# Kernel optimization log

Measured on AMD Instinct MI355X. Metric: run time of the kernel, lower is better.

## Reference

```python
import jax, jax.numpy as jnp
import numpy as np

D = 1024      # hidden_dim
H = 16        # num_heads
KV = 8        # num_kv_heads
HD = D // H   # head_size = 64
M = 3584      # intermediate_dim
E = 8         # num_local_experts
TOPK = 2      # num_experts_per_tok
EPS = 1e-6
ROPE_THETA = 10000.0


def setup_inputs() -> dict:
    key = jax.random.key(0)
    ks = jax.random.split(key, 12)
    s = 0.02
    B, S = 2, 1024
    return {
        "x": jax.random.normal(ks[0], (B, S, D), jnp.float32),
        "ln1_w": jnp.ones((D,), jnp.float32),
        "ln2_w": jnp.ones((D,), jnp.float32),
        "wq": jax.random.normal(ks[1], (D, H * HD), jnp.float32) * s,
        "wk": jax.random.normal(ks[2], (D, KV * HD), jnp.float32) * s,
        "wv": jax.random.normal(ks[3], (D, KV * HD), jnp.float32) * s,
        "wo": jax.random.normal(ks[4], (H * HD, D), jnp.float32) * s,
        "router_w": jax.random.normal(ks[5], (D, E), jnp.float32) * s,
        "w_gate": jax.random.normal(ks[6], (E, D, M), jnp.float32) * s,
        "w_up": jax.random.normal(ks[7], (E, D, M), jnp.float32) * s,
        "w_down": jax.random.normal(ks[8], (E, M, D), jnp.float32) * s,
    }


def _rmsnorm(x, w, eps=EPS):
    xf = x.astype(jnp.float32)
    var = jnp.mean(xf * xf, axis=-1, keepdims=True)
    return (xf * jax.lax.rsqrt(var + eps)).astype(x.dtype) * w


def _rope(q, k):
    # q: [B,S,H,HD], k: [B,S,KV,HD]
    S = q.shape[1]
    inv_freq = 1.0 / (ROPE_THETA ** (jnp.arange(0, HD, 2, dtype=jnp.float32) / HD))
    ang = jnp.arange(S, dtype=jnp.float32)[:, None] * inv_freq[None, :]  # [S, HD/2]
    cos = jnp.concatenate([jnp.cos(ang), jnp.cos(ang)], axis=-1)[None, :, None, :]
    sin = jnp.concatenate([jnp.sin(ang), jnp.sin(ang)], axis=-1)[None, :, None, :]

    def rot_half(t):
        t1, t2 = jnp.split(t, 2, axis=-1)
        return jnp.concatenate([-t2, t1], axis=-1)

    return q * cos + rot_half(q) * sin, k * cos + rot_half(k) * sin


def reference(x, ln1_w, ln2_w, wq, wk, wv, wo, router_w, w_gate, w_up, w_down):
    B, S, _ = x.shape

    # ---- self-attention block ----
    h = _rmsnorm(x, ln1_w)
    q = (h @ wq).reshape(B, S, H, HD)
    k = (h @ wk).reshape(B, S, KV, HD)
    v = (h @ wv).reshape(B, S, KV, HD)
    q, k = _rope(q, k)
    rep = H // KV
    k = jnp.repeat(k, rep, axis=2)  # [B,S,H,HD]
    v = jnp.repeat(v, rep, axis=2)
    scores = jnp.einsum("bqhd,bkhd->bhqk", q, k) / jnp.sqrt(jnp.float32(HD))
    causal = jnp.tril(jnp.ones((S, S), bool))
    scores = jnp.where(causal[None, None], scores, jnp.finfo(scores.dtype).min)
    attn = jax.nn.softmax(scores, axis=-1)
    ao = jnp.einsum("bhqk,bkhd->bqhd", attn, v).reshape(B, S, H * HD)
    x = x + ao @ wo

    # ---- sparse MoE block (top-2 routing, SwiGLU experts) ----
    h = _rmsnorm(x, ln2_w)
    logits = h @ router_w                       # [B,S,E]
    probs = jax.nn.softmax(logits, axis=-1)
    topv, topi = jax.lax.top_k(probs, TOPK)     # [B,S,K]
    topv = topv / jnp.sum(topv, axis=-1, keepdims=True)
    # dense combine weights [B,S,E]: zero for unselected experts
    weights = jnp.sum(jax.nn.one_hot(topi, E, dtype=h.dtype) * topv[..., None], axis=-2)
    gate = jnp.einsum("bsd,edm->bsem", h, w_gate)
    up = jnp.einsum("bsd,edm->bsem", h, w_up)
    act = jax.nn.silu(gate) * up * weights[..., None]
    moe = jnp.einsum("bsem,emd->bsd", act, w_down)
    return x + moe
```

## Files before the change

kernel.cpp:

```cpp
#include <hip/hip_runtime.h>

typedef __attribute__((ext_vector_type(8))) short short8;
typedef __attribute__((ext_vector_type(4))) float f32x4;
typedef unsigned int u32;

#define DI static __device__ __forceinline__

DI unsigned short f2bf(float f) {
  unsigned u = __builtin_bit_cast(unsigned, f);
  u += 0x7fffu + ((u >> 16) & 1u);
  return (unsigned short)(u >> 16);
}
DI float bf2f(unsigned short b) {
  unsigned u = ((unsigned)b) << 16;
  return __builtin_bit_cast(float, u);
}

DI void gload16(const unsigned short* g, unsigned short* l) {
  __builtin_amdgcn_global_load_lds(
      (const __attribute__((address_space(1))) u32*)g,
      (__attribute__((address_space(3))) u32*)l, 16, 0, 0);
}

static constexpr int NT   = 2048;
static constexpr int SEQ  = 1024;
static constexpr int DIM  = 1024;
static constexpr int NH   = 16;
static constexpr int NKV  = 8;
static constexpr int HD   = 64;
static constexpr int MDIM = 3584;
static constexpr int NE   = 8;
static constexpr int QW   = 2048;
static constexpr int GUW  = 2 * MDIM;

template <int ROWMAP>
__global__ void __launch_bounds__(256) transpose_kernel(
    const float* __restrict__ in, unsigned short* __restrict__ out,
    int R, int C, size_t in_estride, size_t out_estride) {
  __shared__ unsigned short tl[64][66];
  int e = blockIdx.z;
  const float* ip = in + (size_t)e * in_estride;
  unsigned short* op = out + (size_t)e * out_estride;
  int c0 = blockIdx.x * 64, r0 = blockIdx.y * 64;
  int tid = threadIdx.x;
  {
    int lr = tid >> 4, lc = (tid & 15) * 4;
#pragma unroll
    for (int p = 0; p < 4; ++p) {
      int r = p * 16 + lr;
      float4 v = *(const float4*)(ip + (size_t)(r0 + r) * C + c0 + lc);
      tl[lc + 0][r] = f2bf(v.x);
      tl[lc + 1][r] = f2bf(v.y);
      tl[lc + 2][r] = f2bf(v.z);
      tl[lc + 3][r] = f2bf(v.w);
    }
  }
  __syncthreads();
  {
    int c = tid >> 2, rc = (tid & 3) * 16;
    unsigned short tmp[16];
#pragma unroll
    for (int j = 0; j < 8; ++j) {
      u32 w = *(const u32*)&tl[c][rc + j * 2];
      tmp[j * 2] = (unsigned short)w;
      tmp[j * 2 + 1] = (unsigned short)(w >> 16);
    }
    int cg = c0 + c;
    int orow;
    if (ROWMAP == 0) orow = cg;
    else orow = ((cg >> 4) << 5) + (cg & 15) + (ROWMAP == 2 ? 16 : 0);
    unsigned short* dst = op + (size_t)orow * R + r0 + rc;
#pragma unroll
    for (int j = 0; j < 2; ++j)
      *(uint4*)(dst + j * 8) = *(const uint4*)&tmp[j * 8];
  }
}

__global__ void __launch_bounds__(256) vtrans_kernel(const unsigned short* __restrict__ qkv,
                                                     unsigned short* __restrict__ vT) {
  __shared__ unsigned short tl[64][66];
  int s0 = blockIdx.x * 64;
  int kvh = blockIdx.y;
  int b = blockIdx.z;
  int tid = threadIdx.x;
  {
    int r = tid >> 2, cc = (tid & 3) * 16;
    const unsigned short* src =
        qkv + ((size_t)(b * SEQ + s0 + r)) * QW + (DIM + NKV * HD + kvh * HD) + cc;
    unsigned short tmp[16];
    *(uint4*)&tmp[0] = *(const uint4*)src;
    *(uint4*)&tmp[8] = *(const uint4*)(src + 8);
#pragma unroll
    for (int j = 0; j < 16; ++j) tl[cc + j][r] = tmp[j];
  }
  __syncthreads();
  {
    int h = tid >> 2, sc = (tid & 3) * 16;
    unsigned short o[16];
#pragma unroll
    for (int j = 0; j < 16; ++j) o[j] = tl[h][sc + j];
    unsigned short* dst = vT + (((size_t)(b * NKV + kvh) * HD + h) * SEQ) + s0 + sc;
    *(uint4*)dst = *(const uint4*)&o[0];
    *(uint4*)(dst + 8) = *(const uint4*)&o[8];
  }
}

__global__ void __launch_bounds__(256) rmsnorm_kernel(const float* __restrict__ x,
                                                      const float* __restrict__ w,
                                                      unsigned short* __restrict__ out) {
  int row = blockIdx.x;
  const float* xr = x + (size_t)row * DIM;
  int i = threadIdx.x * 4;
  float4 v = *(const float4*)(xr + i);
  float s = v.x * v.x + v.y * v.y + v.z * v.z + v.w * v.w;
  for (int o = 32; o; o >>= 1) s += __shfl_xor(s, o);
  __shared__ float red[4];
  if ((threadIdx.x & 63) == 0) red[threadIdx.x >> 6] = s;
  __syncthreads();
  s = red[0] + red[1] + red[2] + red[3];
  float r = rsqrtf(s * (1.0f / DIM) + 1e-6f);
  float4 wv = *(const float4*)(w + i);
  ushort4 o4;
  o4.x = f2bf(v.x * r * wv.x);
  o4.y = f2bf(v.y * r * wv.y);
  o4.z = f2bf(v.z * r * wv.z);
  o4.w = f2bf(v.w * r * wv.w);
  *(ushort4*)(out + (size_t)row * DIM + i) = o4;
}

template <int GATHER, int EPI>
__global__ void __launch_bounds__(256) gemmT_kernel(
    const unsigned short* __restrict__ A, int lda,
    const unsigned short* __restrict__ B, int ldb, size_t b_estride,
    void* __restrict__ Cv, int ldc,
    const float* __restrict__ resid,
    int M, int K,
    const int* __restrict__ lists, const int* __restrict__ cnt,
    int ks_count, size_t ks_stride) {
  constexpr int BN = 128;
  constexpr int NBLK = 2;
  int zz = blockIdx.z;
  int e = zz / ks_count, ks = zz - e * ks_count;
  int KL = K / ks_count;
  int kbase = ks * KL;

  int count = M;
  const int* lst = nullptr;
  if (GATHER != 0) {
    count = cnt[e];
    if (count <= 0) return;
    lst = lists + e * NT;
    B += b_estride * (size_t)e;
  }
  int m0 = blockIdx.y * 128;
  if (m0 >= count) return;
  int n0 = blockIdx.x * BN;

  __shared__ unsigned short sB[3][BN * 32];

  int tid = threadIdx.x, w = tid >> 6, lane = tid & 63;
  int l15 = lane & 15, lhi = lane >> 4;
  int wm = w >> 1, wn = w & 1;

  int srow = w * 16 + (lane >> 2);
  int schunk = (((lane & 3) - ((lane >> 3) & 3)) & 3) * 8;
  const unsigned short* bSrc[NBLK];
#pragma unroll
  for (int s = 0; s < NBLK; ++s)
    bSrc[s] = B + (size_t)(n0 + s * 64 + srow) * ldb + kbase + schunk;
  unsigned ldst = (unsigned)(w * 16) * 32;

  auto stage = [&](int buf, int k0) {
#pragma unroll
    for (int s = 0; s < NBLK; ++s)
      gload16(bSrc[s] + k0, &sB[buf][ldst + s * 64 * 32]);
  };

  const unsigned short* aFrag[4];
#pragma unroll
  for (int mi = 0; mi < 4; ++mi) {
    int mr = m0 + wm * 64 + mi * 16 + l15;
    if (mr > count - 1) mr = count - 1;
    int ar;
    if (GATHER == 0) ar = mr;
    else {
      int pid = lst[mr];
      ar = (GATHER == 1) ? (pid >> 1) : pid;
    }
    aFrag[mi] = A + (size_t)ar * lda + kbase + lhi * 8;
  }

  f32x4 acc[4][4] = {};
  int fslot = ((lhi + (l15 >> 1)) & 3) * 8;
  int boff[4];
#pragma unroll
  for (int t = 0; t < 4; ++t) {
    int col = wn * 64 + t * 16 + l15;
    boff[t] = col * 32 + fslot;
  }

  int nsteps = KL / 32;
  int cur = 0, stg = 2;

  short8 afA[4], afB[4];
  stage(0, 0);
  stage(1, 32);
#pragma unroll
  for (int mi = 0; mi < 4; ++mi) afA[mi] = *(const short8*)(aFrag[mi]);

  auto body = [&](int T, short8(&C)[4], short8(&N)[4]) {
    if (T + 1 < nsteps) asm volatile("s_waitcnt vmcnt(6)" ::: "memory");
    else                asm volatile("s_waitcnt vmcnt(4)" ::: "memory");
    __builtin_amdgcn_s_barrier();
    __builtin_amdgcn_sched_barrier(0);
    int tn = (T + 1 < nsteps) ? T + 1 : T;
#pragma unroll
    for (int mi = 0; mi < 4; ++mi)
      N[mi] = *(const short8*)(aFrag[mi] + (size_t)tn * 32);
    if (T + 2 < nsteps) stage(stg, (T + 2) * 32);
    const unsigned short* pb = sB[cur];
    short8 bfr[4];
#pragma unroll
    for (int q = 0; q < 4; ++q) bfr[q] = *(const short8*)&pb[boff[q]];
    __builtin_amdgcn_s_setprio(1);
#pragma unroll
    for (int mi = 0; mi < 4; ++mi)
#pragma unroll
      for (int ni = 0; ni < 4; ++ni)
        acc[mi][ni] =
            __builtin_amdgcn_mfma_f32_16x16x32_bf16(C[mi], bfr[ni], acc[mi][ni], 0, 0, 0);
    __builtin_amdgcn_s_setprio(0);
    cur = (cur == 2) ? 0 : cur + 1;
    stg = (stg == 2) ? 0 : stg + 1;
  };

  for (int t = 0; t < nsteps; t += 2) {
    body(t, afA, afB);
    body(t + 1, afB, afA);
  }

#pragma unroll
  for (int mi = 0; mi < 4; ++mi) {
#pragma unroll
    for (int r = 0; r < 4; ++r) {
      int mr = m0 + wm * 64 + mi * 16 + lhi * 4 + r;
      if (GATHER != 0 && mr >= count) continue;
      size_t crow = (GATHER != 0) ? (size_t)lst[mr] : (size_t)mr;
      if (EPI == 3) {
        float wgt = resid[crow];
        int colbase = (n0 + wn * 64) >> 1;
#pragma unroll
        for (int ni = 0; ni < 4; ni += 2) {
          float g = acc[mi][ni][r], u = acc[mi][ni + 1][r];
          float sv = g / (1.f + __expf(-g));
          ((unsigned short*)Cv)[crow * ldc + colbase + (ni >> 1) * 16 + l15] =
              f2bf(sv * u * wgt);
        }
      } else {
#pragma unroll
        for (int ni = 0; ni < 4; ++ni) {
          int n = n0 + wn * 64 + ni * 16 + l15;
          float val = acc[mi][ni][r];
          if (EPI == 0)
            ((unsigned short*)Cv)[crow * ldc + n] = f2bf(val);
          else if (EPI == 1)
            ((float*)Cv)[crow * ldc + n] = val + resid[crow * ldc + n];
          else
            ((float*)Cv)[(size_t)ks * ks_stride + crow * ldc + n] = val;
        }
      }
    }
  }
}

__global__ void __launch_bounds__(256) rope_kernel(unsigned short* __restrict__ qkv) {
  int g = blockIdx.x * 256 + threadIdx.x;
  int i = g & 31;
  int hh = (g >> 5) % (NH + NKV);
  int tok = g / (32 * (NH + NKV));
  if (tok >= NT) return;
  int s = tok & (SEQ - 1);
  float inv = exp2f((float)i * (-13.287712379549449f / 32.0f));
  float ang = (float)s * inv;
  float sn = sinf(ang);
  float c = cosf(ang);
  int col = (hh < NH) ? hh * HD : DIM + (hh - NH) * HD;
  unsigned short* ptr = qkv + (size_t)tok * QW + col;
  float a = bf2f(ptr[i]), b2 = bf2f(ptr[i + 32]);
  ptr[i] = f2bf(a * c - b2 * sn);
  ptr[i + 32] = f2bf(b2 * c + a * sn);
}

__global__ void __launch_bounds__(64) attn_kernel(const unsigned short* __restrict__ qkv,
                                                  const unsigned short* __restrict__ vT,
                                                  unsigned short* __restrict__ ao) {
  __shared__ unsigned short Ps[16 * 64];
  int bid = blockIdx.x;
  int qt = bid & 63;
  int h = (bid >> 6) & 15;
  int b = bid >> 10;
  int lane = threadIdx.x, l15 = lane & 15, lhi = lane >> 4;
  int q0 = qt * 16, kvh = h >> 1;
  int kcol = DIM + kvh * HD;

  const unsigned short* qp = qkv + ((size_t)(b * SEQ + q0 + l15)) * QW + h * HD + lhi * 8;
  short8 aq0 = *(const short8*)qp;
  short8 aq1 = *(const short8*)(qp + 32);

  const unsigned short* vbase = vT + ((size_t)(b * NKV + kvh) * HD) * SEQ;

  float m[4] = {-1e30f, -1e30f, -1e30f, -1e30f};
  float l[4] = {0.f, 0.f, 0.f, 0.f};
  f32x4 accO[4] = {};

  int nkb = (qt >> 2) + 1;
  for (int kb_ = 0; kb_ < nkb; ++kb_) {
    int kbase = kb_ * 64;
    f32x4 s[4];
#pragma unroll
    for (int ct = 0; ct < 4; ++ct) {
      const unsigned short* kp =
          qkv + ((size_t)(b * SEQ + kbase + ct * 16 + l15)) * QW + kcol + lhi * 8;
      short8 k0v = *(const short8*)kp;
      short8 k1v = *(const short8*)(kp + 32);
      f32x4 a = {};
      a = __builtin_amdgcn_mfma_f32_16x16x32_bf16(aq0, k0v, a, 0, 0, 0);
      a = __builtin_amdgcn_mfma_f32_16x16x32_bf16(aq1, k1v, a, 0, 0, 0);
      int kpos = kbase + ct * 16 + l15;
#pragma unroll
      for (int r = 0; r < 4; ++r) {
        float v = a[r] * 0.125f;
        if (kpos > q0 + lhi * 4 + r) v = -1e30f;
        s[ct][r] = v;
      }
    }
    float nm[4], al[4], rs[4];
#pragma unroll
    for (int r = 0; r < 4; ++r) {
      float mb = fmaxf(fmaxf(s[0][r], s[1][r]), fmaxf(s[2][r], s[3][r]));
      mb = fmaxf(mb, __shfl_xor(mb, 1));
      mb = fmaxf(mb, __shfl_xor(mb, 2));
      mb = fmaxf(mb, __shfl_xor(mb, 4));
      mb = fmaxf(mb, __shfl_xor(mb, 8));
      nm[r] = fmaxf(m[r], mb);
      al[r] = __expf(m[r] - nm[r]);
      m[r] = nm[r];
      rs[r] = 0.f;
    }
#pragma unroll
    for (int ct = 0; ct < 4; ++ct) {
#pragma unroll
      for (int r = 0; r < 4; ++r) {
        float p = __expf(s[ct][r] - nm[r]);
        rs[r] += p;
        int q = lhi * 4 + r;
        Ps[q * 64 + ((ct * 16 + l15) ^ (lhi << 4))] = f2bf(p);
      }
    }
#pragma unroll
    for (int r = 0; r < 4; ++r) {
      rs[r] += __shfl_xor(rs[r], 1);
      rs[r] += __shfl_xor(rs[r], 2);
      rs[r] += __shfl_xor(rs[r], 4);
      rs[r] += __shfl_xor(rs[r], 8);
      l[r] = l[r] * al[r] + rs[r];
    }
#pragma unroll
    for (int dt = 0; dt < 4; ++dt)
#pragma unroll
      for (int r = 0; r < 4; ++r) accO[dt][r] *= al[r];

    int pswz = (l15 >> 2) << 4;
    short8 ap0 = *(const short8*)&Ps[l15 * 64 + ((lhi * 8) ^ pswz)];
    short8 ap1 = *(const short8*)&Ps[l15 * 64 + ((32 + lhi * 8) ^ pswz)];
#pragma unroll
    for (int dt = 0; dt < 4; ++dt) {
#pragma unroll
      for (int ks = 0; ks < 2; ++ks) {
        const unsigned short* vp =
            vbase + ((size_t)(dt * 16 + l15)) * SEQ + kbase + ks * 32 + lhi * 8;
        short8 vf = *(const short8*)vp;
        accO[dt] = __builtin_amdgcn_mfma_f32_16x16x32_bf16(ks ? ap1 : ap0, vf, accO[dt], 0, 0, 0);
      }
    }
  }
  float invl[4];
#pragma unroll
  for (int r = 0; r < 4; ++r) invl[r] = 1.f / l[r];
#pragma unroll
  for (int dt = 0; dt < 4; ++dt)
#pragma unroll
    for (int r = 0; r < 4; ++r)
      ao[((size_t)(b * SEQ + q0 + lhi * 4 + r)) * DIM + h * HD + dt * 16 + l15] =
          f2bf(accO[dt][r] * invl[r]);
}

__global__ void zero_cnt_kernel(int* __restrict__ cnt) {
  if (threadIdx.x < NE) cnt[threadIdx.x] = 0;
}

__global__ void __launch_bounds__(64) router_kernel(const float* __restrict__ x2,
                                                    const float* __restrict__ ln2w,
                                                    const float* __restrict__ rw,
                                                    float* __restrict__ wts,
                                                    int* __restrict__ cnt,
                                                    int* __restrict__ lists) {
  int t = blockIdx.x, lane = threadIdx.x;
  const float* xr = x2 + (size_t)t * DIM;
  float xs[16];
  double ssq = 0.0;
#pragma unroll
  for (int j = 0; j < 16; ++j) {
    xs[j] = xr[lane + j * 64];
    ssq += (double)xs[j] * xs[j];
  }
  for (int o = 32; o; o >>= 1) ssq += __shfl_xor(ssq, o);
  double r = rsqrt(ssq * (1.0 / DIM) + 1e-6);
  double p[NE] = {};
#pragma unroll
  for (int j = 0; j < 16; ++j) {
    int i = lane + j * 64;
    double hv = (double)xs[j] * r * (double)ln2w[i];
    const float* rwp = rw + (size_t)i * NE;
#pragma unroll
    for (int e = 0; e < NE; ++e) p[e] += hv * (double)rwp[e];
  }
  for (int o = 32; o; o >>= 1) {
#pragma unroll
    for (int e = 0; e < NE; ++e) p[e] += __shfl_xor(p[e], o);
  }
  if (lane == 0) {
    int i1 = 0;
    for (int e = 1; e < NE; ++e)
      if (p[e] > p[i1]) i1 = e;
    int i2 = (i1 == 0) ? 1 : 0;
    for (int e = 0; e < NE; ++e)
      if (e != i1 && p[e] > p[i2]) i2 = e;
    double mx = fmax(p[i1], p[i2]);
    double e1 = exp(p[i1] - mx), e2 = exp(p[i2] - mx);
    double inv = 1.0 / (e1 + e2);
    wts[t * 2] = (float)(e1 * inv);
    wts[t * 2 + 1] = (float)(e2 * inv);
    int pos1 = atomicAdd(&cnt[i1], 1);
    lists[i1 * NT + pos1] = t * 2;
    int pos2 = atomicAdd(&cnt[i2], 1);
    lists[i2 * NT + pos2] = t * 2 + 1;
  }
}

__global__ void __launch_bounds__(256) combine_kernel(const float* __restrict__ x2,
                                                      const float* __restrict__ part,
                                                      float* __restrict__ out) {
  const size_t KSS = (size_t)2 * NT * DIM;
  size_t idx = ((size_t)blockIdx.x * 256 + threadIdx.x) * 4;
  size_t t = idx >> 10;
  size_t d = idx & 1023;
  float4 o = *(const float4*)(x2 + idx);
#pragma unroll
  for (int s = 0; s < 4; ++s) {
    float4 b0 = *(const float4*)(part + s * KSS + (t * 2) * DIM + d);
    float4 c0 = *(const float4*)(part + s * KSS + (t * 2 + 1) * DIM + d);
    o.x += b0.x + c0.x;
    o.y += b0.y + c0.y;
    o.z += b0.z + c0.z;
    o.w += b0.w + c0.w;
  }
  *(float4*)(out + idx) = o;
}

extern "C" void kernel_launch(void* const* d_in, const int* in_sizes, int n_in,
                              void* d_out, int out_size, void* d_ws, size_t ws_size,
                              hipStream_t stream) {
  const float* x   = (const float*)d_in[0];
  const float* ln1 = (const float*)d_in[1];
  const float* ln2 = (const float*)d_in[2];
  const float* wq  = (const float*)d_in[3];
  const float* wk  = (const float*)d_in[4];
  const float* wv  = (const float*)d_in[5];
  const float* wo  = (const float*)d_in[6];
  const float* rw  = (const float*)d_in[7];
  const float* wg  = (const float*)d_in[8];
  const float* wu  = (const float*)d_in[9];
  const float* wd  = (const float*)d_in[10];
  float* out = (float*)d_out;

  char* p = (char*)d_ws;
  auto take = [&](size_t bytes) {
    char* q = p;
    p += (bytes + 255) & ~(size_t)255;
    return q;
  };
  unsigned short* wguT = (unsigned short*)take((size_t)NE * GUW * DIM * 2);
  unsigned short* wdT  = (unsigned short*)take((size_t)NE * DIM * MDIM * 2);
  float*          x2   = (float*)take((size_t)NT * DIM * 4);
  unsigned short* h2   = (unsigned short*)take((size_t)NT * DIM * 2);
  float*          part = (float*)take((size_t)4 * 2 * NT * DIM * 4);
  unsigned short* act  = (unsigned short*)take((size_t)2 * NT * MDIM * 2);
  float*          wtsb = (float*)take((size_t)2 * NT * 4);
  int*            cntb = (int*)take(NE * 4);
  int*            listsb = (int*)take((size_t)NE * NT * 4);
  char* X = p;
  unsigned short* wqkvT = (unsigned short*)X;
  unsigned short* woT   = wqkvT + (size_t)QW * DIM;
  unsigned short* h1    = woT + (size_t)DIM * DIM;
  unsigned short* qkv   = h1 + (size_t)NT * DIM;
  unsigned short* aob   = qkv + (size_t)NT * QW;
  unsigned short* vT    = aob + (size_t)NT * DIM;

  transpose_kernel<0><<<dim3(16, 16, 1), 256, 0, stream>>>(wq, wqkvT, DIM, DIM, 0, 0);
  transpose_kernel<0><<<dim3(8, 16, 1), 256, 0, stream>>>(wk, wqkvT + (size_t)DIM * DIM, DIM, 512, 0, 0);
  transpose_kernel<0><<<dim3(8, 16, 1), 256, 0, stream>>>(wv, wqkvT + (size_t)(DIM + 512) * DIM, DIM, 512, 0, 0);
  transpose_kernel<0><<<dim3(16, 16, 1), 256, 0, stream>>>(wo, woT, DIM, DIM, 0, 0);
  transpose_kernel<1><<<dim3(56, 16, NE), 256, 0, stream>>>(
      wg, wguT, DIM, MDIM, (size_t)DIM * MDIM, (size_t)GUW * DIM);
  transpose_kernel<2><<<dim3(56, 16, NE), 256, 0, stream>>>(
      wu, wguT, DIM, MDIM, (size_t)DIM * MDIM, (size_t)GUW * DIM);
  transpose_kernel<0><<<dim3(16, 56, NE), 256, 0, stream>>>(
      wd, wdT, MDIM, DIM, (size_t)MDIM * DIM, (size_t)DIM * MDIM);

  rmsnorm_kernel<<<NT, 256, 0, stream>>>(x, ln1, h1);
  gemmT_kernel<0, 0><<<dim3(QW / 128, NT / 128, 1), 256, 0, stream>>>(
      h1, DIM, wqkvT, DIM, 0, qkv, QW, nullptr, NT, DIM, nullptr, nullptr, 1, 0);
  rope_kernel<<<(NT * (NH + NKV) * 32) / 256, 256, 0, stream>>>(qkv);
  vtrans_kernel<<<dim3(SEQ / 64, NKV, 2), 256, 0, stream>>>(qkv, vT);
  attn_kernel<<<NT * NH / 16, 64, 0, stream>>>(qkv, vT, aob);
  gemmT_kernel<0, 1><<<dim3(DIM / 128, NT / 128, 1), 256, 0, stream>>>(
      aob, DIM, woT, DIM, 0, x2, DIM, x, NT, DIM, nullptr, nullptr, 1, 0);

  rmsnorm_kernel<<<NT, 256, 0, stream>>>(x2, ln2, h2);
  zero_cnt_kernel<<<1, 64, 0, stream>>>(cntb);
  router_kernel<<<NT, 64, 0, stream>>>(x2, ln2, rw, wtsb, cntb, listsb);

  gemmT_kernel<1, 3><<<dim3(GUW / 128, 16, NE), 256, 0, stream>>>(
      h2, DIM, wguT, DIM, (size_t)GUW * DIM, act, MDIM, wtsb, 0, DIM, listsb, cntb, 1, 0);
  gemmT_kernel<2, 2><<<dim3(DIM / 128, 16, NE * 4), 256, 0, stream>>>(
      act, MDIM, wdT, MDIM, (size_t)DIM * MDIM, part, DIM, nullptr, 0, MDIM, listsb, cntb,
      4, (size_t)2 * NT * DIM);

  combine_kernel<<<(NT * DIM) / 1024, 256, 0, stream>>>(x2, part, out);
}
```

Before: 613.9 us.

## Stage A tiles through LDS and use 256-row tiles for MoE GEMMs

The GEMM kernel now loads A tiles into LDS with async global-to-LDS loads, in a triple buffer alongside B, instead of having each wave read A fragments directly from global memory into registers. The M tile size becomes a template parameter. The MoE gate/up and down GEMMs use 256-row tiles, with 8 accumulator rows per wave, to reuse each expert's weight tiles across more tokens. The cost is more LDS use, more accumulator registers and lower occupancy, plus fewer blocks when tokens are spread unevenly across experts.

```diff
diff --git a/kernel.cpp b/kernel.cpp
--- a/kernel.cpp
+++ b/kernel.cpp
@@ -128,7 +128,7 @@
   *(ushort4*)(out + (size_t)row * DIM + i) = o4;
 }
 
-template <int GATHER, int EPI>
+template <int GATHER, int EPI, int WM>
 __global__ void __launch_bounds__(256) gemmT_kernel(
     const unsigned short* __restrict__ A, int lda,
     const unsigned short* __restrict__ B, int ldb, size_t b_estride,
@@ -137,8 +137,8 @@
     int M, int K,
     const int* __restrict__ lists, const int* __restrict__ cnt,
     int ks_count, size_t ks_stride) {
-  constexpr int BN = 128;
-  constexpr int NBLK = 2;
+  constexpr int BM = WM * 32;
+  constexpr int ABLK = BM / 64;
   int zz = blockIdx.z;
   int e = zz / ks_count, ks = zz - e * ks_count;
   int KL = K / ks_count;
@@ -152,11 +152,12 @@
     lst = lists + e * NT;
     B += b_estride * (size_t)e;
   }
-  int m0 = blockIdx.y * 128;
+  int m0 = blockIdx.y * BM;
   if (m0 >= count) return;
-  int n0 = blockIdx.x * BN;
-
-  __shared__ unsigned short sB[3][BN * 32];
+  int n0 = blockIdx.x * 128;
+
+  __shared__ unsigned short sA[3][BM * 32];
+  __shared__ unsigned short sB[3][128 * 32];
 
   int tid = threadIdx.x, w = tid >> 6, lane = tid & 63;
   int l15 = lane & 15, lhi = lane >> 4;
@@ -164,22 +165,11 @@
 
   int srow = w * 16 + (lane >> 2);
   int schunk = (((lane & 3) - ((lane >> 3) & 3)) & 3) * 8;
-  const unsigned short* bSrc[NBLK];
-#pragma unroll
-  for (int s = 0; s < NBLK; ++s)
-    bSrc[s] = B + (size_t)(n0 + s * 64 + srow) * ldb + kbase + schunk;
-  unsigned ldst = (unsigned)(w * 16) * 32;
-
-  auto stage = [&](int buf, int k0) {
-#pragma unroll
-    for (int s = 0; s < NBLK; ++s)
-      gload16(bSrc[s] + k0, &sB[buf][ldst + s * 64 * 32]);
-  };
-
-  const unsigned short* aFrag[4];
-#pragma unroll
-  for (int mi = 0; mi < 4; ++mi) {
-    int mr = m0 + wm * 64 + mi * 16 + l15;
+  const unsigned short* aSrc[ABLK];
+  const unsigned short* bSrc[2];
+#pragma unroll
+  for (int s = 0; s < ABLK; ++s) {
+    int mr = m0 + s * 64 + srow;
     if (mr > count - 1) mr = count - 1;
     int ar;
     if (GATHER == 0) ar = mr;
@@ -187,12 +177,30 @@
       int pid = lst[mr];
       ar = (GATHER == 1) ? (pid >> 1) : pid;
     }
-    aFrag[mi] = A + (size_t)ar * lda + kbase + lhi * 8;
-  }
-
-  f32x4 acc[4][4] = {};
+    aSrc[s] = A + (size_t)ar * lda + kbase + schunk;
+  }
+#pragma unroll
+  for (int s = 0; s < 2; ++s)
+    bSrc[s] = B + (size_t)(n0 + s * 64 + srow) * ldb + kbase + schunk;
+  unsigned ldst = (unsigned)(w * 16) * 32;
+
+  auto stage = [&](int buf, int k0) {
+#pragma unroll
+    for (int s = 0; s < ABLK; ++s)
+      gload16(aSrc[s] + k0, &sA[buf][ldst + s * 64 * 32]);
+#pragma unroll
+    for (int s = 0; s < 2; ++s)
+      gload16(bSrc[s] + k0, &sB[buf][ldst + s * 64 * 32]);
+  };
+
+  f32x4 acc[WM][4] = {};
   int fslot = ((lhi + (l15 >> 1)) & 3) * 8;
-  int boff[4];
+  int aoff[WM], boff[4];
+#pragma unroll
+  for (int t = 0; t < WM; ++t) {
+    int row = wm * (BM / 2) + t * 16 + l15;
+    aoff[t] = row * 32 + fslot;
+  }
 #pragma unroll
   for (int t = 0; t < 4; ++t) {
     int col = wn * 64 + t * 16 + l15;
@@ -200,50 +208,44 @@
   }
 
   int nsteps = KL / 32;
+  stage(0, 0);
+  if (nsteps > 1) stage(1, 32);
+
   int cur = 0, stg = 2;
-
-  short8 afA[4], afB[4];
-  stage(0, 0);
-  stage(1, 32);
-#pragma unroll
-  for (int mi = 0; mi < 4; ++mi) afA[mi] = *(const short8*)(aFrag[mi]);
-
-  auto body = [&](int T, short8(&C)[4], short8(&N)[4]) {
-    if (T + 1 < nsteps) asm volatile("s_waitcnt vmcnt(6)" ::: "memory");
-    else                asm volatile("s_waitcnt vmcnt(4)" ::: "memory");
+  for (int t = 0; t < nsteps; ++t) {
+    if (t + 1 < nsteps) {
+      if constexpr (WM == 8) asm volatile("s_waitcnt vmcnt(6)" ::: "memory");
+      else                   asm volatile("s_waitcnt vmcnt(4)" ::: "memory");
+    } else {
+      asm volatile("s_waitcnt vmcnt(0)" ::: "memory");
+    }
     __builtin_amdgcn_s_barrier();
     __builtin_amdgcn_sched_barrier(0);
-    int tn = (T + 1 < nsteps) ? T + 1 : T;
-#pragma unroll
-    for (int mi = 0; mi < 4; ++mi)
-      N[mi] = *(const short8*)(aFrag[mi] + (size_t)tn * 32);
-    if (T + 2 < nsteps) stage(stg, (T + 2) * 32);
+    if (t + 2 < nsteps) stage(stg, (t + 2) * 32);
+    const unsigned short* pa = sA[cur];
     const unsigned short* pb = sB[cur];
     short8 bfr[4];
 #pragma unroll
     for (int q = 0; q < 4; ++q) bfr[q] = *(const short8*)&pb[boff[q]];
     __builtin_amdgcn_s_setprio(1);
 #pragma unroll
-    for (int mi = 0; mi < 4; ++mi)
+    for (int mi = 0; mi < WM; ++mi) {
+      short8 af = *(const short8*)&pa[aoff[mi]];
 #pragma unroll
       for (int ni = 0; ni < 4; ++ni)
         acc[mi][ni] =
-            __builtin_amdgcn_mfma_f32_16x16x32_bf16(C[mi], bfr[ni], acc[mi][ni], 0, 0, 0);
+            __builtin_amdgcn_mfma_f32_16x16x32_bf16(af, bfr[ni], acc[mi][ni], 0, 0, 0);
+    }
     __builtin_amdgcn_s_setprio(0);
     cur = (cur == 2) ? 0 : cur + 1;
     stg = (stg == 2) ? 0 : stg + 1;
-  };
-
-  for (int t = 0; t < nsteps; t += 2) {
-    body(t, afA, afB);
-    body(t + 1, afB, afA);
-  }
-
-#pragma unroll
-  for (int mi = 0; mi < 4; ++mi) {
+  }
+
+#pragma unroll
+  for (int mi = 0; mi < WM; ++mi) {
 #pragma unroll
     for (int r = 0; r < 4; ++r) {
-      int mr = m0 + wm * 64 + mi * 16 + lhi * 4 + r;
+      int mr = m0 + wm * (BM / 2) + mi * 16 + lhi * 4 + r;
       if (GATHER != 0 && mr >= count) continue;
       size_t crow = (GATHER != 0) ? (size_t)lst[mr] : (size_t)mr;
       if (EPI == 3) {
@@ -519,21 +521,21 @@
       wd, wdT, MDIM, DIM, (size_t)MDIM * DIM, (size_t)DIM * MDIM);
 
   rmsnorm_kernel<<<NT, 256, 0, stream>>>(x, ln1, h1);
-  gemmT_kernel<0, 0><<<dim3(QW / 128, NT / 128, 1), 256, 0, stream>>>(
+  gemmT_kernel<0, 0, 4><<<dim3(QW / 128, NT / 128, 1), 256, 0, stream>>>(
       h1, DIM, wqkvT, DIM, 0, qkv, QW, nullptr, NT, DIM, nullptr, nullptr, 1, 0);
   rope_kernel<<<(NT * (NH + NKV) * 32) / 256, 256, 0, stream>>>(qkv);
   vtrans_kernel<<<dim3(SEQ / 64, NKV, 2), 256, 0, stream>>>(qkv, vT);
   attn_kernel<<<NT * NH / 16, 64, 0, stream>>>(qkv, vT, aob);
-  gemmT_kernel<0, 1><<<dim3(DIM / 128, NT / 128, 1), 256, 0, stream>>>(
+  gemmT_kernel<0, 1, 4><<<dim3(DIM / 128, NT / 128, 1), 256, 0, stream>>>(
       aob, DIM, woT, DIM, 0, x2, DIM, x, NT, DIM, nullptr, nullptr, 1, 0);
 
   rmsnorm_kernel<<<NT, 256, 0, stream>>>(x2, ln2, h2);
   zero_cnt_kernel<<<1, 64, 0, stream>>>(cntb);
   router_kernel<<<NT, 64, 0, stream>>>(x2, ln2, rw, wtsb, cntb, listsb);
 
-  gemmT_kernel<1, 3><<<dim3(GUW / 128, 16, NE), 256, 0, stream>>>(
+  gemmT_kernel<1, 3, 8><<<dim3(GUW / 128, 8, NE), 256, 0, stream>>>(
       h2, DIM, wguT, DIM, (size_t)GUW * DIM, act, MDIM, wtsb, 0, DIM, listsb, cntb, 1, 0);
-  gemmT_kernel<2, 2><<<dim3(DIM / 128, 16, NE * 4), 256, 0, stream>>>(
+  gemmT_kernel<2, 2, 8><<<dim3(DIM / 128, 8, NE * 4), 256, 0, stream>>>(
       act, MDIM, wdT, MDIM, (size_t)DIM * MDIM, part, DIM, nullptr, 0, MDIM, listsb, cntb,
       4, (size_t)2 * NT * DIM);
 
```

Measured after the change: 629.7 us. 2.6% more time.
